# Performance work log

Measured on AMD Instinct MI355X. Metric: run time of the kernel, lower is better.

## Reference

```python
import jax, jax.numpy as jnp
import numpy as np

N_NODES = 50000
N_EDGES = 1600000
D = 128  # in_dim = hidden = out_dim = 128


def _gat_layer(x, W, b, aW, ab, src, dst, n_nodes):
    # fc: z = x @ W^T + b   (torch Linear convention, W:[out,in])
    z = x @ W.T + b                      # [N, d]
    d = z.shape[1]
    # attn_fc(concat(z_src, z_dst)) decomposed into per-node halves
    a_src = z @ aW[0, :d]                # [N]
    a_dst = z @ aW[0, d:]                # [N]
    e = jax.nn.leaky_relu(a_src[src] + a_dst[dst] + ab[0])  # [E], slope 0.01 (torch default)
    # segment softmax over incoming edges of each dst node
    m = jax.ops.segment_max(e, dst, num_segments=n_nodes)   # [N]
    ex = jnp.exp(e - m[dst])             # [E]
    s = jax.ops.segment_sum(ex, dst, num_segments=n_nodes)  # [N]
    alpha = ex / s[dst]                  # [E]
    # weighted scatter-sum of source features
    h = jax.ops.segment_sum(alpha[:, None] * z[src], dst, num_segments=n_nodes)  # [N, d]
    return h


def setup_inputs() -> dict:
    key = jax.random.key(0)
    ks = jax.random.split(key, 16)
    x = jax.random.normal(ks[0], (N_NODES, D), dtype=jnp.float32)
    src = jax.random.randint(ks[1], (N_EDGES,), 0, N_NODES, dtype=jnp.int32)
    dst = jax.random.randint(ks[2], (N_EDGES,), 0, N_NODES, dtype=jnp.int32)
    inp = {"x": x, "src": src, "dst": dst, "t": 0}
    # 3 GAT layers (128->128, 128->128, 128->128); xavier-ish scale
    for i in range(3):
        base = 3 + 4 * i
        inp[f"W{i}"] = jax.random.normal(ks[base], (D, D), dtype=jnp.float32) * (1.0 / np.sqrt(D))
        inp[f"b{i}"] = jnp.zeros((D,), dtype=jnp.float32)
        inp[f"aW{i}"] = jax.random.normal(ks[base + 1], (1, 2 * D), dtype=jnp.float32) * (1.0 / np.sqrt(2 * D))
        inp[f"ab{i}"] = jnp.zeros((1,), dtype=jnp.float32)
    return inp


def reference(x, src, dst, t, W0, b0, aW0, ab0, W1, b1, aW1, ab1, W2, b2, aW2, ab2):
    n = x.shape[0]
    h = _gat_layer(x, W0, b0, aW0, ab0, src, dst, n)
    h = jax.nn.relu(h)
    h = _gat_layer(h, W1, b1, aW1, ab1, src, dst, n)
    h = jax.nn.relu(h)
    h = _gat_layer(h, W2, b2, aW2, ab2, src, dst, n)
    return h
```

## Files before the change

### kernel.cpp

```cpp
#include <hip/hip_runtime.h>
#include <hip/hip_fp16.h>
#include <math.h>

#define DD 128
#define NBKT 391
#define P1CHUNK 4096
#define P2CAP 8192


__global__ __launch_bounds__(256) void fill_zero_i(int* p, int n) {
    int i = blockIdx.x * 256 + threadIdx.x;
    if (i < n) p[i] = 0;
}


__global__ __launch_bounds__(512) void p1hist_k(const int* __restrict__ dst, int* __restrict__ gcount, int E) {
    __shared__ int lh[NBKT];
    const int tid = threadIdx.x;
    for (int i = tid; i < NBKT; i += 512) lh[i] = 0;
    __syncthreads();
    const int blk0 = blockIdx.x * P1CHUNK;
    const int blkE = min(blk0 + P1CHUNK, E);
    int i0 = blk0 + tid * 8;
    if (i0 + 8 <= blkE) {
        int4 d0 = *reinterpret_cast<const int4*>(dst + i0);
        int4 d1 = *reinterpret_cast<const int4*>(dst + i0 + 4);
        atomicAdd(&lh[d0.x >> 7], 1); atomicAdd(&lh[d0.y >> 7], 1);
        atomicAdd(&lh[d0.z >> 7], 1); atomicAdd(&lh[d0.w >> 7], 1);
        atomicAdd(&lh[d1.x >> 7], 1); atomicAdd(&lh[d1.y >> 7], 1);
        atomicAdd(&lh[d1.z >> 7], 1); atomicAdd(&lh[d1.w >> 7], 1);
    } else {
        for (int j = 0; j < 8; ++j) {
            int i = i0 + j;
            if (i < blkE) atomicAdd(&lh[dst[i] >> 7], 1);
        }
    }
    __syncthreads();
    for (int i = tid; i < NBKT; i += 512)
        if (lh[i]) atomicAdd(&gcount[i], lh[i]);
}


__global__ __launch_bounds__(512) void p1scan_k(const int* __restrict__ gcount, int* __restrict__ bbase,
                                                int* __restrict__ bcur, int E) {
    __shared__ int tmp[512];
    int t = threadIdx.x;
    int v = (t < NBKT) ? gcount[t] : 0;
    tmp[t] = v;
    __syncthreads();
#pragma unroll
    for (int o = 1; o < 512; o <<= 1) {
        int add = (t >= o) ? tmp[t - o] : 0;
        __syncthreads();
        tmp[t] += add;
        __syncthreads();
    }
    if (t <= NBKT) {
        int ex = (t < NBKT) ? (tmp[t] - v) : E;
        bbase[t] = ex;
        if (t < NBKT) bcur[t] = ex;
    }
}


__global__ __launch_bounds__(512) void p1scatter_k(const int* __restrict__ src, const int* __restrict__ dst,
                                                   int* __restrict__ bcur, int2* __restrict__ bufA, int E) {
    __shared__ int lcnt[NBKT];
    __shared__ int lstart[512];
    __shared__ int blkb[NBKT];
    __shared__ int2 stage[P1CHUNK];
    const int tid = threadIdx.x;
    for (int i = tid; i < NBKT; i += 512) lcnt[i] = 0;
    __syncthreads();
    const int blk0 = blockIdx.x * P1CHUNK;
    const int blkE = min(blk0 + P1CHUNK, E);
    const int i0 = blk0 + tid * 8;

    int sv[8], dv[8], bn[8], rk[8], cntT = 0;
    if (i0 + 8 <= blkE) {
        int4 s0 = *reinterpret_cast<const int4*>(src + i0);
        int4 s1 = *reinterpret_cast<const int4*>(src + i0 + 4);
        int4 d0 = *reinterpret_cast<const int4*>(dst + i0);
        int4 d1 = *reinterpret_cast<const int4*>(dst + i0 + 4);
        sv[0] = s0.x; sv[1] = s0.y; sv[2] = s0.z; sv[3] = s0.w;
        sv[4] = s1.x; sv[5] = s1.y; sv[6] = s1.z; sv[7] = s1.w;
        dv[0] = d0.x; dv[1] = d0.y; dv[2] = d0.z; dv[3] = d0.w;
        dv[4] = d1.x; dv[5] = d1.y; dv[6] = d1.z; dv[7] = d1.w;
        cntT = 8;
    } else {
#pragma unroll
        for (int j = 0; j < 8; ++j) {
            int i = i0 + j;
            if (i < blkE) { sv[j] = src[i]; dv[j] = dst[i]; cntT = j + 1; }
        }
    }
#pragma unroll
    for (int j = 0; j < 8; ++j) {
        if (j < cntT) {
            bn[j] = dv[j] >> 7;
            rk[j] = atomicAdd(&lcnt[bn[j]], 1);
        }
    }
    __syncthreads();
    int v = (tid < NBKT) ? lcnt[tid] : 0;
    lstart[tid] = v;
    __syncthreads();
#pragma unroll
    for (int o = 1; o < 512; o <<= 1) {
        int add = (tid >= o) ? lstart[tid - o] : 0;
        __syncthreads();
        lstart[tid] += add;
        __syncthreads();
    }
    lstart[tid] -= v;
    __syncthreads();
    for (int i = tid; i < NBKT; i += 512)
        blkb[i] = lcnt[i] ? atomicAdd(&bcur[i], lcnt[i]) : 0;
#pragma unroll
    for (int j = 0; j < 8; ++j) {
        if (j < cntT) {
            int pos = lstart[bn[j]] + rk[j];
            stage[pos] = make_int2(sv[j], dv[j]);
        }
    }
    __syncthreads();
    const int cnt = blkE - blk0;
    for (int j = tid; j < cnt; j += 512) {
        int2 e = stage[j];
        int b = e.y >> 7;
        bufA[blkb[b] + (j - lstart[b])] = e;
    }
}


__global__ __launch_bounds__(512) void p2sort_k(const int2* __restrict__ bufA, const int* __restrict__ bbase,
                                                int* __restrict__ srcs, int* __restrict__ dstS) {
    __shared__ int h2[128];
    __shared__ int start2[128];
    __shared__ int cur2[128];
    __shared__ int ssrc[P2CAP];
    __shared__ int sdst[P2CAP];
    const int tid = threadIdx.x;
    const int b = blockIdx.x;
    const int base = bbase[b];
    const int cnt = bbase[b + 1] - base;
    for (int i = tid; i < 128; i += 512) h2[i] = 0;
    __syncthreads();
    for (int j = tid; j < cnt; j += 512)
        atomicAdd(&h2[bufA[base + j].y & 127], 1);
    __syncthreads();
    if (tid == 0) {
        int s = 0;
        for (int i = 0; i < 128; ++i) { start2[i] = s; cur2[i] = s; s += h2[i]; }
    }
    __syncthreads();
    for (int j = tid; j < cnt; j += 512) {
        int2 e = bufA[base + j];
        int p = atomicAdd(&cur2[e.y & 127], 1);
        ssrc[p] = e.x;
        sdst[p] = e.y;
    }
    __syncthreads();
    for (int j = tid; j < cnt; j += 512) {
        srcs[base + j] = ssrc[j];
        dstS[base + j] = sdst[j];
    }
}


__global__ __launch_bounds__(512) void off_k(const int* __restrict__ dstS, int* __restrict__ off, int N, int E) {
    int i = blockIdx.x * 512 + threadIdx.x;
    if (i >= E) return;
    int d = dstS[i];
    int p = (i == 0) ? -1 : dstS[i - 1];
    if (d != p)
        for (int n = p + 1; n <= d; ++n) off[n] = i;
    if (i == E - 1)
        for (int n = d + 1; n <= N; ++n) off[n] = E;
}


__global__ __launch_bounds__(512) void gemm_k(const float* __restrict__ X, const float* __restrict__ W,
                                              const float* __restrict__ B, const float* __restrict__ aW,
                                              __half* __restrict__ Zh, float* __restrict__ a_src,
                                              float* __restrict__ a_dst, int N) {
    __shared__ __align__(16) float xs[32][128];
    __shared__ __align__(16) float ws[32][128];
    const int tid = threadIdx.x;
    const int row0 = blockIdx.x * 128;
    const int cg = tid & 31;
    const int rg = tid >> 5;
    float acc[8][4];
#pragma unroll
    for (int i = 0; i < 8; ++i)
#pragma unroll
        for (int j = 0; j < 4; ++j) acc[i][j] = 0.f;

    for (int kc = 0; kc < DD; kc += 32) {
        {
            int r = tid >> 2;
            int k4 = (tid & 3) * 8;
            int gr = row0 + r;
            if (gr >= N) gr = N - 1;
            const float4* p = reinterpret_cast<const float4*>(X + (size_t)gr * DD + kc + k4);
            float4 v0 = p[0], v1 = p[1];
            xs[k4 + 0][r] = v0.x; xs[k4 + 1][r] = v0.y; xs[k4 + 2][r] = v0.z; xs[k4 + 3][r] = v0.w;
            xs[k4 + 4][r] = v1.x; xs[k4 + 5][r] = v1.y; xs[k4 + 6][r] = v1.z; xs[k4 + 7][r] = v1.w;
        }
        {
            int o = tid >> 2;
            int k8 = (tid & 3) * 8;
            const float4* p = reinterpret_cast<const float4*>(W + (size_t)o * DD + kc + k8);
            float4 v0 = p[0], v1 = p[1];
            ws[k8 + 0][o] = v0.x; ws[k8 + 1][o] = v0.y; ws[k8 + 2][o] = v0.z; ws[k8 + 3][o] = v0.w;
            ws[k8 + 4][o] = v1.x; ws[k8 + 5][o] = v1.y; ws[k8 + 6][o] = v1.z; ws[k8 + 7][o] = v1.w;
        }
        __syncthreads();
#pragma unroll
        for (int k = 0; k < 32; ++k) {
            const float4 wv = *reinterpret_cast<const float4*>(&ws[k][cg * 4]);
            const float4 xa = *reinterpret_cast<const float4*>(&xs[k][rg * 8]);
            const float4 xb = *reinterpret_cast<const float4*>(&xs[k][rg * 8 + 4]);
            float xr[8] = {xa.x, xa.y, xa.z, xa.w, xb.x, xb.y, xb.z, xb.w};
            float wr[4] = {wv.x, wv.y, wv.z, wv.w};
#pragma unroll
            for (int i = 0; i < 8; ++i)
#pragma unroll
                for (int j = 0; j < 4; ++j)
                    acc[i][j] = fmaf(xr[i], wr[j], acc[i][j]);
        }
        __syncthreads();
    }
    const int c0 = cg * 4;
    const float4 bv = *reinterpret_cast<const float4*>(B + c0);
    const float4 aw0 = *reinterpret_cast<const float4*>(aW + c0);
    const float4 aw1 = *reinterpret_cast<const float4*>(aW + DD + c0);
    float pa[8], pb[8];
#pragma unroll
    for (int i = 0; i < 8; ++i) {
        acc[i][0] += bv.x; acc[i][1] += bv.y; acc[i][2] += bv.z; acc[i][3] += bv.w;
        pa[i] = acc[i][0] * aw0.x + acc[i][1] * aw0.y + acc[i][2] * aw0.z + acc[i][3] * aw0.w;
        pb[i] = acc[i][0] * aw1.x + acc[i][1] * aw1.y + acc[i][2] * aw1.z + acc[i][3] * aw1.w;
    }
#pragma unroll
    for (int o = 1; o < 32; o <<= 1) {
#pragma unroll
        for (int i = 0; i < 8; ++i) {
            pa[i] += __shfl_xor(pa[i], o);
            pb[i] += __shfl_xor(pb[i], o);
        }
    }
    const int sl = c0 >> 5;
    const int cin = c0 & 31;
#pragma unroll
    for (int i = 0; i < 8; ++i) {
        int gr = row0 + rg * 8 + i;
        if (gr < N) {
            __half2 p0 = __floats2half2_rn(acc[i][0], acc[i][1]);
            __half2 p1 = __floats2half2_rn(acc[i][2], acc[i][3]);
            __half2* dst2 = reinterpret_cast<__half2*>(Zh + ((size_t)sl * N + gr) * 32 + cin);
            dst2[0] = p0;
            dst2[1] = p1;
            if (cg == 0) {
                a_src[gr] = pa[i];
                a_dst[gr] = pb[i];
            }
        }
    }
}


__global__ __launch_bounds__(256) void alpha_k(const float* __restrict__ a_src, const float* __restrict__ a_dst,
                                               const int* __restrict__ off, const int* __restrict__ srcs,
                                               const float* __restrict__ ab, unsigned* __restrict__ pairc, int N) {
    int node = blockIdx.x * 4 + (threadIdx.x >> 6);
    int lane = threadIdx.x & 63;
    if (node >= N) return;
    const int beg = off[node], end = off[node + 1];
    const int deg = end - beg;
    const float adn = a_dst[node] + ab[0];
    if (deg <= 64) {
        int i = beg + lane;
        float p = 0.f; int s = 0;
        if (i < end) {
            s = srcs[i];
            float e = a_src[s] + adn;
            e = (e > 0.f) ? e : 0.01f * e;
            p = __expf(e);
        }
        float psum = p;
#pragma unroll
        for (int o = 1; o < 64; o <<= 1) psum += __shfl_xor(psum, o);
        float inv = (deg > 0) ? 1.0f / psum : 0.0f;
        if (i < end) {
            unsigned ah = __half_as_ushort(__float2half(p * inv));
            pairc[i] = (ah << 16) | (unsigned)s;
        }
    } else {
        float psum = 0.f;
        for (int i = beg + lane; i < end; i += 64) {
            float e = a_src[srcs[i]] + adn;
            e = (e > 0.f) ? e : 0.01f * e;
            psum += __expf(e);
        }
#pragma unroll
        for (int o = 1; o < 64; o <<= 1) psum += __shfl_xor(psum, o);
        const float inv = 1.0f / psum;
        for (int i = beg + lane; i < end; i += 64) {
            int s = srcs[i];
            float e = a_src[s] + adn;
            e = (e > 0.f) ? e : 0.01f * e;
            unsigned ah = __half_as_ushort(__float2half(__expf(e) * inv));
            pairc[i] = (ah << 16) | (unsigned)s;
        }
    }
}


__global__ __launch_bounds__(256) void aggr_k(const __half* __restrict__ Zh, const unsigned* __restrict__ pairc,
                                              const int* __restrict__ off, float* __restrict__ H,
                                              int N, int do_relu) {
    const int slice = blockIdx.x & 3;
    const int lane = threadIdx.x & 63;
    const int wid = threadIdx.x >> 6;
    const int ng = lane >> 4;
    const int node = (blockIdx.x >> 2) * 16 + wid * 4 + ng;
    if (node >= N) return;
    const int eg = (lane >> 2) & 3;
    const int ql = lane & 3;
    const int beg = off[node], end = off[node + 1];
    const __half* Zs = Zh + (size_t)slice * N * 32 + ql * 8;

    float acc[8];
#pragma unroll
    for (int k = 0; k < 8; ++k) acc[k] = 0.f;

    int i = beg + eg;
    for (; i + 4 < end; i += 8) {
        unsigned w0 = pairc[i];
        unsigned w1 = pairc[i + 4];
        int s0 = (int)(w0 & 0xffffu);
        int s1 = (int)(w1 & 0xffffu);
        float a0 = __half2float(__ushort_as_half((unsigned short)(w0 >> 16)));
        float a1 = __half2float(__ushort_as_half((unsigned short)(w1 >> 16)));
        int4 r0 = *reinterpret_cast<const int4*>(Zs + (size_t)s0 * 32);
        int4 r1 = *reinterpret_cast<const int4*>(Zs + (size_t)s1 * 32);
        const __half* h0 = reinterpret_cast<const __half*>(&r0);
        const __half* h1 = reinterpret_cast<const __half*>(&r1);
#pragma unroll
        for (int k = 0; k < 8; ++k) acc[k] = fmaf(a0, __half2float(h0[k]), acc[k]);
#pragma unroll
        for (int k = 0; k < 8; ++k) acc[k] = fmaf(a1, __half2float(h1[k]), acc[k]);
    }
    if (i < end) {
        unsigned w0 = pairc[i];
        int s0 = (int)(w0 & 0xffffu);
        float a0 = __half2float(__ushort_as_half((unsigned short)(w0 >> 16)));
        int4 r0 = *reinterpret_cast<const int4*>(Zs + (size_t)s0 * 32);
        const __half* h0 = reinterpret_cast<const __half*>(&r0);
#pragma unroll
        for (int k = 0; k < 8; ++k) acc[k] = fmaf(a0, __half2float(h0[k]), acc[k]);
    }
#pragma unroll
    for (int o = 4; o <= 8; o <<= 1) {
#pragma unroll
        for (int k = 0; k < 8; ++k) acc[k] += __shfl_xor(acc[k], o);
    }
    if (eg == 0) {
#pragma unroll
        for (int k = 0; k < 8; ++k)
            if (do_relu) acc[k] = fmaxf(acc[k], 0.f);
        float* out = H + (size_t)node * DD + slice * 32 + ql * 8;
#pragma unroll
        for (int k = 0; k < 8; ++k)
            __builtin_nontemporal_store(acc[k], out + k);
    }
}


extern "C" void kernel_launch(void* const* d_in, const int* in_sizes, int n_in,
                              void* d_out, int out_size, void* d_ws, size_t ws_size,
                              hipStream_t stream) {
    const float* x  = (const float*)d_in[0];
    const int* src  = (const int*)d_in[1];
    const int* dst  = (const int*)d_in[2];
    const float* Wl[3]  = {(const float*)d_in[4],  (const float*)d_in[8],  (const float*)d_in[12]};
    const float* bl[3]  = {(const float*)d_in[5],  (const float*)d_in[9],  (const float*)d_in[13]};
    const float* aWl[3] = {(const float*)d_in[6],  (const float*)d_in[10], (const float*)d_in[14]};
    const float* abl[3] = {(const float*)d_in[7],  (const float*)d_in[11], (const float*)d_in[15]};
    const int N = in_sizes[0] / DD;
    const int E = in_sizes[1];

    char* p = (char*)d_ws;
    auto alloc = [&](size_t bytes) -> char* {
        char* r = p;
        p += (bytes + 255) & ~(size_t)255;
        return r;
    };
    __half* zh  = (__half*)alloc((size_t)N * DD * 2);
    float* hA   = (float*)alloc((size_t)N * DD * 4);
    float* hB   = (float*)alloc((size_t)N * DD * 4);
    float* asrc = (float*)alloc((size_t)N * 4);
    float* adst = (float*)alloc((size_t)N * 4);
    int* off    = (int*)alloc((size_t)(N + 1) * 4);
    int* srcs   = (int*)alloc((size_t)E * 4);
    unsigned* pairc = (unsigned*)alloc((size_t)E * 4);
    int* gcount = (int*)alloc(512 * 4);
    int* bbase  = (int*)alloc(512 * 4);
    int* bcur   = (int*)alloc(512 * 4);
    int2* bufA  = (int2*)hB;
    int* dstS   = (int*)hA;

    const int NBLK1 = (E + P1CHUNK - 1) / P1CHUNK;

    fill_zero_i<<<2, 256, 0, stream>>>(gcount, 512);
    p1hist_k<<<NBLK1, 512, 0, stream>>>(dst, gcount, E);
    p1scan_k<<<1, 512, 0, stream>>>(gcount, bbase, bcur, E);
    p1scatter_k<<<NBLK1, 512, 0, stream>>>(src, dst, bcur, bufA, E);
    p2sort_k<<<NBKT, 512, 0, stream>>>(bufA, bbase, srcs, dstS);
    off_k<<<(E + 511) / 512, 512, 0, stream>>>(dstS, off, N, E);

    const float* in = x;
    float* outs[3] = {hA, hB, (float*)d_out};
    const int node_blocks = (N + 3) / 4;
    const int aggr_blocks = 4 * ((N + 15) / 16);
    for (int l = 0; l < 3; ++l) {
        gemm_k<<<(N + 127) / 128, 512, 0, stream>>>(in, Wl[l], bl[l], aWl[l], zh, asrc, adst, N);
        alpha_k<<<node_blocks, 256, 0, stream>>>(asrc, adst, off, srcs, abl[l], pairc, N);
        aggr_k<<<aggr_blocks, 256, 0, stream>>>(zh, pairc, off, outs[l], N, (l < 2) ? 1 : 0);
        in = outs[l];
    }
}
```

Measured before the change: 314.2 us.

## Fuse offset computation into bucket sort and widen per-lane edge unroll in aggregation

The CSR offset computation moves into the second-stage sort kernel, which derives each node's offsets from the shared-memory sorted destinations. This removes the separate off_k launch and the global round trip of the sorted-destination array. Separately, the aggregation kernel now gives each node 8 lanes (2 edge groups) instead of 16 (4 edge groups) and issues four gathers per iteration. That doubles nodes per block, raises memory-level parallelism per lane and needs only one shuffle-reduction step, at the cost of more serial work per lane for high-degree nodes.

```diff
diff --git a/kernel.cpp b/kernel.cpp
--- a/kernel.cpp
+++ b/kernel.cpp
@@ -134,9 +134,8 @@
 
 
 __global__ __launch_bounds__(512) void p2sort_k(const int2* __restrict__ bufA, const int* __restrict__ bbase,
-                                                int* __restrict__ srcs, int* __restrict__ dstS) {
+                                                int* __restrict__ srcs, int* __restrict__ off, int N, int E) {
     __shared__ int h2[128];
-    __shared__ int start2[128];
     __shared__ int cur2[128];
     __shared__ int ssrc[P2CAP];
     __shared__ int sdst[P2CAP];
@@ -151,7 +150,7 @@
     __syncthreads();
     if (tid == 0) {
         int s = 0;
-        for (int i = 0; i < 128; ++i) { start2[i] = s; cur2[i] = s; s += h2[i]; }
+        for (int i = 0; i < 128; ++i) { cur2[i] = s; s += h2[i]; }
     }
     __syncthreads();
     for (int j = tid; j < cnt; j += 512) {
@@ -161,22 +160,19 @@
         sdst[p] = e.y;
     }
     __syncthreads();
+    const int n0 = b * 128;
+    const int n1 = min(n0 + 128, N);
     for (int j = tid; j < cnt; j += 512) {
         srcs[base + j] = ssrc[j];
-        dstS[base + j] = sdst[j];
-    }
-}
-
-
-__global__ __launch_bounds__(512) void off_k(const int* __restrict__ dstS, int* __restrict__ off, int N, int E) {
-    int i = blockIdx.x * 512 + threadIdx.x;
-    if (i >= E) return;
-    int d = dstS[i];
-    int p = (i == 0) ? -1 : dstS[i - 1];
-    if (d != p)
-        for (int n = p + 1; n <= d; ++n) off[n] = i;
-    if (i == E - 1)
-        for (int n = d + 1; n <= N; ++n) off[n] = E;
+        int d = sdst[j];
+        int p = (j == 0) ? (n0 - 1) : sdst[j - 1];
+        for (int n = p + 1; n <= d; ++n) off[n] = base + j;
+        if (j == cnt - 1)
+            for (int n = d + 1; n < n1; ++n) off[n] = base + cnt;
+    }
+    if (cnt == 0)
+        for (int n = n0 + tid; n < n1; n += 512) off[n] = base;
+    if (b == NBKT - 1 && tid == 0) off[N] = E;
 }
 
 
@@ -323,10 +319,10 @@
     const int slice = blockIdx.x & 3;
     const int lane = threadIdx.x & 63;
     const int wid = threadIdx.x >> 6;
-    const int ng = lane >> 4;
-    const int node = (blockIdx.x >> 2) * 16 + wid * 4 + ng;
+    const int ng = lane >> 3;
+    const int node = (blockIdx.x >> 2) * 32 + wid * 8 + ng;
     if (node >= N) return;
-    const int eg = (lane >> 2) & 3;
+    const int eg = (lane >> 2) & 1;
     const int ql = lane & 3;
     const int beg = off[node], end = off[node + 1];
     const __half* Zs = Zh + (size_t)slice * N * 32 + ql * 8;
@@ -336,23 +332,37 @@
     for (int k = 0; k < 8; ++k) acc[k] = 0.f;
 
     int i = beg + eg;
-    for (; i + 4 < end; i += 8) {
+    for (; i + 6 < end; i += 8) {
         unsigned w0 = pairc[i];
-        unsigned w1 = pairc[i + 4];
+        unsigned w1 = pairc[i + 2];
+        unsigned w2 = pairc[i + 4];
+        unsigned w3 = pairc[i + 6];
         int s0 = (int)(w0 & 0xffffu);
         int s1 = (int)(w1 & 0xffffu);
+        int s2 = (int)(w2 & 0xffffu);
+        int s3 = (int)(w3 & 0xffffu);
+        int4 r0 = *reinterpret_cast<const int4*>(Zs + (size_t)s0 * 32);
+        int4 r1 = *reinterpret_cast<const int4*>(Zs + (size_t)s1 * 32);
+        int4 r2 = *reinterpret_cast<const int4*>(Zs + (size_t)s2 * 32);
+        int4 r3 = *reinterpret_cast<const int4*>(Zs + (size_t)s3 * 32);
         float a0 = __half2float(__ushort_as_half((unsigned short)(w0 >> 16)));
         float a1 = __half2float(__ushort_as_half((unsigned short)(w1 >> 16)));
-        int4 r0 = *reinterpret_cast<const int4*>(Zs + (size_t)s0 * 32);
-        int4 r1 = *reinterpret_cast<const int4*>(Zs + (size_t)s1 * 32);
+        float a2 = __half2float(__ushort_as_half((unsigned short)(w2 >> 16)));
+        float a3 = __half2float(__ushort_as_half((unsigned short)(w3 >> 16)));
         const __half* h0 = reinterpret_cast<const __half*>(&r0);
         const __half* h1 = reinterpret_cast<const __half*>(&r1);
+        const __half* h2 = reinterpret_cast<const __half*>(&r2);
+        const __half* h3 = reinterpret_cast<const __half*>(&r3);
 #pragma unroll
         for (int k = 0; k < 8; ++k) acc[k] = fmaf(a0, __half2float(h0[k]), acc[k]);
 #pragma unroll
         for (int k = 0; k < 8; ++k) acc[k] = fmaf(a1, __half2float(h1[k]), acc[k]);
-    }
-    if (i < end) {
+#pragma unroll
+        for (int k = 0; k < 8; ++k) acc[k] = fmaf(a2, __half2float(h2[k]), acc[k]);
+#pragma unroll
+        for (int k = 0; k < 8; ++k) acc[k] = fmaf(a3, __half2float(h3[k]), acc[k]);
+    }
+    for (; i < end; i += 2) {
         unsigned w0 = pairc[i];
         int s0 = (int)(w0 & 0xffffu);
         float a0 = __half2float(__ushort_as_half((unsigned short)(w0 >> 16)));
@@ -362,10 +372,7 @@
         for (int k = 0; k < 8; ++k) acc[k] = fmaf(a0, __half2float(h0[k]), acc[k]);
     }
 #pragma unroll
-    for (int o = 4; o <= 8; o <<= 1) {
-#pragma unroll
-        for (int k = 0; k < 8; ++k) acc[k] += __shfl_xor(acc[k], o);
-    }
+    for (int k = 0; k < 8; ++k) acc[k] += __shfl_xor(acc[k], 4);
     if (eg == 0) {
 #pragma unroll
         for (int k = 0; k < 8; ++k)
@@ -409,7 +416,6 @@
     int* bbase  = (int*)alloc(512 * 4);
     int* bcur   = (int*)alloc(512 * 4);
     int2* bufA  = (int2*)hB;
-    int* dstS   = (int*)hA;
 
     const int NBLK1 = (E + P1CHUNK - 1) / P1CHUNK;
 
@@ -417,13 +423,12 @@
     p1hist_k<<<NBLK1, 512, 0, stream>>>(dst, gcount, E);
     p1scan_k<<<1, 512, 0, stream>>>(gcount, bbase, bcur, E);
     p1scatter_k<<<NBLK1, 512, 0, stream>>>(src, dst, bcur, bufA, E);
-    p2sort_k<<<NBKT, 512, 0, stream>>>(bufA, bbase, srcs, dstS);
-    off_k<<<(E + 511) / 512, 512, 0, stream>>>(dstS, off, N, E);
+    p2sort_k<<<NBKT, 512, 0, stream>>>(bufA, bbase, srcs, off, N, E);
 
     const float* in = x;
     float* outs[3] = {hA, hB, (float*)d_out};
     const int node_blocks = (N + 3) / 4;
-    const int aggr_blocks = 4 * ((N + 15) / 16);
+    const int aggr_blocks = 4 * ((N + 31) / 32);
     for (int l = 0; l < 3; ++l) {
         gemm_k<<<(N + 127) / 128, 512, 0, stream>>>(in, Wl[l], bl[l], aWl[l], zh, asrc, adst, N);
         alpha_k<<<node_blocks, 256, 0, stream>>>(asrc, adst, off, srcs, abl[l], pairc, N);
```

After: 312.8 us. Within noise of the previous version (-0.4%).

## Use fp16 MFMA GEMM with half activations and fuse offset build into sort

Applied to the files above, without the earlier changes.

The FP32 SIMT GEMM is replaced with an fp16 MFMA 16x16x32 kernel. Inputs are converted to half by new conversion kernels, and the intermediate layer outputs are now stored as half with ReLU fused in. The separate off_k kernel is removed: p2sort_k computes node offsets directly from its sorted shared buffer, which also drops the dstS global write. This cuts GEMM compute time and intermediate memory traffic, at the cost of lower precision in the inputs and activations and some extra conversion launches.

```diff
diff --git a/kernel.cpp b/kernel.cpp
--- a/kernel.cpp
+++ b/kernel.cpp
@@ -7,10 +7,45 @@
 #define P1CHUNK 4096
 #define P2CAP 8192
 
+typedef _Float16 half8 __attribute__((ext_vector_type(8)));
+typedef float floatx4 __attribute__((ext_vector_type(4)));
+
 
 __global__ __launch_bounds__(256) void fill_zero_i(int* p, int n) {
     int i = blockIdx.x * 256 + threadIdx.x;
     if (i < n) p[i] = 0;
+}
+
+
+__global__ __launch_bounds__(256) void cvt_k(const float* __restrict__ X, __half* __restrict__ Xh, int n8) {
+    int i = blockIdx.x * 256 + threadIdx.x;
+    if (i >= n8) return;
+    const float4* p = reinterpret_cast<const float4*>(X + (size_t)i * 8);
+    float4 v0 = p[0], v1 = p[1];
+    __half hv[8];
+    hv[0] = __float2half(v0.x); hv[1] = __float2half(v0.y);
+    hv[2] = __float2half(v0.z); hv[3] = __float2half(v0.w);
+    hv[4] = __float2half(v1.x); hv[5] = __float2half(v1.y);
+    hv[6] = __float2half(v1.z); hv[7] = __float2half(v1.w);
+    *reinterpret_cast<int4*>(Xh + (size_t)i * 8) = *reinterpret_cast<const int4*>(hv);
+}
+
+__global__ __launch_bounds__(256) void cvtw3_k(const float* __restrict__ W0, const float* __restrict__ W1,
+                                               const float* __restrict__ W2, __half* __restrict__ Wh3) {
+    int i = blockIdx.x * 256 + threadIdx.x;
+    if (i >= 2048) return;
+    const float* Ws[3] = {W0, W1, W2};
+#pragma unroll
+    for (int m = 0; m < 3; ++m) {
+        const float4* p = reinterpret_cast<const float4*>(Ws[m] + (size_t)i * 8);
+        float4 v0 = p[0], v1 = p[1];
+        __half hv[8];
+        hv[0] = __float2half(v0.x); hv[1] = __float2half(v0.y);
+        hv[2] = __float2half(v0.z); hv[3] = __float2half(v0.w);
+        hv[4] = __float2half(v1.x); hv[5] = __float2half(v1.y);
+        hv[6] = __float2half(v1.z); hv[7] = __float2half(v1.w);
+        *reinterpret_cast<int4*>(Wh3 + (size_t)m * 16384 + (size_t)i * 8) = *reinterpret_cast<const int4*>(hv);
+    }
 }
 
 
@@ -134,9 +169,8 @@
 
 
 __global__ __launch_bounds__(512) void p2sort_k(const int2* __restrict__ bufA, const int* __restrict__ bbase,
-                                                int* __restrict__ srcs, int* __restrict__ dstS) {
+                                                int* __restrict__ srcs, int* __restrict__ off, int N, int E) {
     __shared__ int h2[128];
-    __shared__ int start2[128];
     __shared__ int cur2[128];
     __shared__ int ssrc[P2CAP];
     __shared__ int sdst[P2CAP];
@@ -151,7 +185,7 @@
     __syncthreads();
     if (tid == 0) {
         int s = 0;
-        for (int i = 0; i < 128; ++i) { start2[i] = s; cur2[i] = s; s += h2[i]; }
+        for (int i = 0; i < 128; ++i) { cur2[i] = s; s += h2[i]; }
     }
     __syncthreads();
     for (int j = tid; j < cnt; j += 512) {
@@ -161,109 +195,85 @@
         sdst[p] = e.y;
     }
     __syncthreads();
+    const int n0 = b * 128;
+    const int n1 = min(n0 + 128, N);
     for (int j = tid; j < cnt; j += 512) {
         srcs[base + j] = ssrc[j];
-        dstS[base + j] = sdst[j];
-    }
-}
-
-
-__global__ __launch_bounds__(512) void off_k(const int* __restrict__ dstS, int* __restrict__ off, int N, int E) {
-    int i = blockIdx.x * 512 + threadIdx.x;
-    if (i >= E) return;
-    int d = dstS[i];
-    int p = (i == 0) ? -1 : dstS[i - 1];
-    if (d != p)
-        for (int n = p + 1; n <= d; ++n) off[n] = i;
-    if (i == E - 1)
-        for (int n = d + 1; n <= N; ++n) off[n] = E;
-}
-
-
-__global__ __launch_bounds__(512) void gemm_k(const float* __restrict__ X, const float* __restrict__ W,
+        int d = sdst[j];
+        int p = (j == 0) ? (n0 - 1) : sdst[j - 1];
+        for (int n = p + 1; n <= d; ++n) off[n] = base + j;
+        if (j == cnt - 1)
+            for (int n = d + 1; n < n1; ++n) off[n] = base + cnt;
+    }
+    if (cnt == 0)
+        for (int n = n0 + tid; n < n1; n += 512) off[n] = base;
+    if (b == NBKT - 1 && tid == 0) off[N] = E;
+}
+
+
+__global__ __launch_bounds__(256) void gemm_k(const __half* __restrict__ Xh, const __half* __restrict__ Wh,
                                               const float* __restrict__ B, const float* __restrict__ aW,
                                               __half* __restrict__ Zh, float* __restrict__ a_src,
                                               float* __restrict__ a_dst, int N) {
-    __shared__ __align__(16) float xs[32][128];
-    __shared__ __align__(16) float ws[32][128];
     const int tid = threadIdx.x;
-    const int row0 = blockIdx.x * 128;
-    const int cg = tid & 31;
-    const int rg = tid >> 5;
-    float acc[8][4];
-#pragma unroll
-    for (int i = 0; i < 8; ++i)
-#pragma unroll
-        for (int j = 0; j < 4; ++j) acc[i][j] = 0.f;
-
-    for (int kc = 0; kc < DD; kc += 32) {
-        {
-            int r = tid >> 2;
-            int k4 = (tid & 3) * 8;
-            int gr = row0 + r;
-            if (gr >= N) gr = N - 1;
-            const float4* p = reinterpret_cast<const float4*>(X + (size_t)gr * DD + kc + k4);
-            float4 v0 = p[0], v1 = p[1];
-            xs[k4 + 0][r] = v0.x; xs[k4 + 1][r] = v0.y; xs[k4 + 2][r] = v0.z; xs[k4 + 3][r] = v0.w;
-            xs[k4 + 4][r] = v1.x; xs[k4 + 5][r] = v1.y; xs[k4 + 6][r] = v1.z; xs[k4 + 7][r] = v1.w;
-        }
-        {
-            int o = tid >> 2;
-            int k8 = (tid & 3) * 8;
-            const float4* p = reinterpret_cast<const float4*>(W + (size_t)o * DD + kc + k8);
-            float4 v0 = p[0], v1 = p[1];
-            ws[k8 + 0][o] = v0.x; ws[k8 + 1][o] = v0.y; ws[k8 + 2][o] = v0.z; ws[k8 + 3][o] = v0.w;
-            ws[k8 + 4][o] = v1.x; ws[k8 + 5][o] = v1.y; ws[k8 + 6][o] = v1.z; ws[k8 + 7][o] = v1.w;
-        }
-        __syncthreads();
-#pragma unroll
-        for (int k = 0; k < 32; ++k) {
-            const float4 wv = *reinterpret_cast<const float4*>(&ws[k][cg * 4]);
-            const float4 xa = *reinterpret_cast<const float4*>(&xs[k][rg * 8]);
-            const float4 xb = *reinterpret_cast<const float4*>(&xs[k][rg * 8 + 4]);
-            float xr[8] = {xa.x, xa.y, xa.z, xa.w, xb.x, xb.y, xb.z, xb.w};
-            float wr[4] = {wv.x, wv.y, wv.z, wv.w};
-#pragma unroll
-            for (int i = 0; i < 8; ++i)
-#pragma unroll
-                for (int j = 0; j < 4; ++j)
-                    acc[i][j] = fmaf(xr[i], wr[j], acc[i][j]);
-        }
-        __syncthreads();
-    }
-    const int c0 = cg * 4;
-    const float4 bv = *reinterpret_cast<const float4*>(B + c0);
-    const float4 aw0 = *reinterpret_cast<const float4*>(aW + c0);
-    const float4 aw1 = *reinterpret_cast<const float4*>(aW + DD + c0);
-    float pa[8], pb[8];
-#pragma unroll
-    for (int i = 0; i < 8; ++i) {
-        acc[i][0] += bv.x; acc[i][1] += bv.y; acc[i][2] += bv.z; acc[i][3] += bv.w;
-        pa[i] = acc[i][0] * aw0.x + acc[i][1] * aw0.y + acc[i][2] * aw0.z + acc[i][3] * aw0.w;
-        pb[i] = acc[i][0] * aw1.x + acc[i][1] * aw1.y + acc[i][2] * aw1.z + acc[i][3] * aw1.w;
-    }
-#pragma unroll
-    for (int o = 1; o < 32; o <<= 1) {
-#pragma unroll
-        for (int i = 0; i < 8; ++i) {
-            pa[i] += __shfl_xor(pa[i], o);
-            pb[i] += __shfl_xor(pb[i], o);
-        }
-    }
-    const int sl = c0 >> 5;
-    const int cin = c0 & 31;
-#pragma unroll
-    for (int i = 0; i < 8; ++i) {
-        int gr = row0 + rg * 8 + i;
-        if (gr < N) {
-            __half2 p0 = __floats2half2_rn(acc[i][0], acc[i][1]);
-            __half2 p1 = __floats2half2_rn(acc[i][2], acc[i][3]);
-            __half2* dst2 = reinterpret_cast<__half2*>(Zh + ((size_t)sl * N + gr) * 32 + cin);
-            dst2[0] = p0;
-            dst2[1] = p1;
-            if (cg == 0) {
-                a_src[gr] = pa[i];
-                a_dst[gr] = pb[i];
+    const int wid = tid >> 6;
+    const int lane = tid & 63;
+    const int cl = lane & 15;
+    const int kg = lane >> 4;
+    const int row0 = blockIdx.x * 64 + wid * 16;
+    int rowA = row0 + cl;
+    if (rowA >= N) rowA = N - 1;
+
+    floatx4 acc[8];
+#pragma unroll
+    for (int t = 0; t < 8; ++t) acc[t] = {0.f, 0.f, 0.f, 0.f};
+
+    const _Float16* Xp = reinterpret_cast<const _Float16*>(Xh);
+    const _Float16* Wp = reinterpret_cast<const _Float16*>(Wh);
+#pragma unroll
+    for (int kk = 0; kk < 4; ++kk) {
+        const int kb = kk * 32 + kg * 8;
+        half8 av = *reinterpret_cast<const half8*>(Xp + (size_t)rowA * 128 + kb);
+#pragma unroll
+        for (int t = 0; t < 8; ++t) {
+            half8 bv = *reinterpret_cast<const half8*>(Wp + (size_t)(t * 16 + cl) * 128 + kb);
+            acc[t] = __builtin_amdgcn_mfma_f32_16x16x32_f16(av, bv, acc[t], 0, 0, 0);
+        }
+    }
+    float pa[4] = {0.f, 0.f, 0.f, 0.f}, pb[4] = {0.f, 0.f, 0.f, 0.f};
+#pragma unroll
+    for (int t = 0; t < 8; ++t) {
+        const int c = t * 16 + cl;
+        const float bc = B[c];
+        const float w0 = aW[c];
+        const float w1 = aW[128 + c];
+        const int sl = c >> 5;
+        const int cin = c & 31;
+#pragma unroll
+        for (int j = 0; j < 4; ++j) {
+            float z = acc[t][j] + bc;
+            pa[j] = fmaf(z, w0, pa[j]);
+            pb[j] = fmaf(z, w1, pb[j]);
+            int grow = row0 + kg * 4 + j;
+            if (grow < N)
+                Zh[((size_t)sl * N + grow) * 32 + cin] = __float2half(z);
+        }
+    }
+#pragma unroll
+    for (int o = 1; o < 16; o <<= 1) {
+#pragma unroll
+        for (int j = 0; j < 4; ++j) {
+            pa[j] += __shfl_xor(pa[j], o);
+            pb[j] += __shfl_xor(pb[j], o);
+        }
+    }
+    if (cl == 0) {
+#pragma unroll
+        for (int j = 0; j < 4; ++j) {
+            int grow = row0 + kg * 4 + j;
+            if (grow < N) {
+                a_src[grow] = pa[j];
+                a_dst[grow] = pb[j];
             }
         }
     }
@@ -318,8 +328,8 @@
 
 
 __global__ __launch_bounds__(256) void aggr_k(const __half* __restrict__ Zh, const unsigned* __restrict__ pairc,
-                                              const int* __restrict__ off, float* __restrict__ H,
-                                              int N, int do_relu) {
+                                              const int* __restrict__ off, float* __restrict__ Hf,
+                                              __half* __restrict__ Hh, int N) {
     const int slice = blockIdx.x & 3;
     const int lane = threadIdx.x & 63;
     const int wid = threadIdx.x >> 6;
@@ -367,13 +377,18 @@
         for (int k = 0; k < 8; ++k) acc[k] += __shfl_xor(acc[k], o);
     }
     if (eg == 0) {
-#pragma unroll
-        for (int k = 0; k < 8; ++k)
-            if (do_relu) acc[k] = fmaxf(acc[k], 0.f);
-        float* out = H + (size_t)node * DD + slice * 32 + ql * 8;
-#pragma unroll
-        for (int k = 0; k < 8; ++k)
-            __builtin_nontemporal_store(acc[k], out + k);
+        if (Hh) {
+            __half hv[8];
+#pragma unroll
+            for (int k = 0; k < 8; ++k) hv[k] = __float2half(fmaxf(acc[k], 0.f));
+            *reinterpret_cast<int4*>(Hh + (size_t)node * DD + slice * 32 + ql * 8) =
+                *reinterpret_cast<const int4*>(hv);
+        } else {
+            float* out = Hf + (size_t)node * DD + slice * 32 + ql * 8;
+#pragma unroll
+            for (int k = 0; k < 8; ++k)
+                __builtin_nontemporal_store(acc[k], out + k);
+        }
     }
 }
 
@@ -397,9 +412,10 @@
         p += (bytes + 255) & ~(size_t)255;
         return r;
     };
+    __half* Wh3 = (__half*)alloc(3 * 16384 * 2);
+    __half* XhA = (__half*)alloc((size_t)N * DD * 2);
+    __half* XhB = (__half*)alloc((size_t)N * DD * 2);
     __half* zh  = (__half*)alloc((size_t)N * DD * 2);
-    float* hA   = (float*)alloc((size_t)N * DD * 4);
-    float* hB   = (float*)alloc((size_t)N * DD * 4);
     float* asrc = (float*)alloc((size_t)N * 4);
     float* adst = (float*)alloc((size_t)N * 4);
     int* off    = (int*)alloc((size_t)(N + 1) * 4);
@@ -408,8 +424,7 @@
     int* gcount = (int*)alloc(512 * 4);
     int* bbase  = (int*)alloc(512 * 4);
     int* bcur   = (int*)alloc(512 * 4);
-    int2* bufA  = (int2*)hB;
-    int* dstS   = (int*)hA;
+    int2* bufA  = (int2*)alloc((size_t)E * 8);
 
     const int NBLK1 = (E + P1CHUNK - 1) / P1CHUNK;
 
@@ -417,17 +432,22 @@
     p1hist_k<<<NBLK1, 512, 0, stream>>>(dst, gcount, E);
     p1scan_k<<<1, 512, 0, stream>>>(gcount, bbase, bcur, E);
     p1scatter_k<<<NBLK1, 512, 0, stream>>>(src, dst, bcur, bufA, E);
-    p2sort_k<<<NBKT, 512, 0, stream>>>(bufA, bbase, srcs, dstS);
-    off_k<<<(E + 511) / 512, 512, 0, stream>>>(dstS, off, N, E);
-
-    const float* in = x;
-    float* outs[3] = {hA, hB, (float*)d_out};
+    p2sort_k<<<NBKT, 512, 0, stream>>>(bufA, bbase, srcs, off, N, E);
+    cvtw3_k<<<8, 256, 0, stream>>>(Wl[0], Wl[1], Wl[2], Wh3);
+    const int n8 = N * DD / 8;
+    cvt_k<<<(n8 + 255) / 256, 256, 0, stream>>>(x, XhA, n8);
+
     const int node_blocks = (N + 3) / 4;
     const int aggr_blocks = 4 * ((N + 15) / 16);
+    const int gemm_blocks = (N + 63) / 64;
+
+    __half* xin[3]  = {XhA, XhB, XhA};
+    __half* hout[3] = {XhB, XhA, nullptr};
     for (int l = 0; l < 3; ++l) {
-        gemm_k<<<(N + 127) / 128, 512, 0, stream>>>(in, Wl[l], bl[l], aWl[l], zh, asrc, adst, N);
+        gemm_k<<<gemm_blocks, 256, 0, stream>>>(xin[l], Wh3 + (size_t)l * 16384, bl[l], aWl[l],
+                                                zh, asrc, adst, N);
         alpha_k<<<node_blocks, 256, 0, stream>>>(asrc, adst, off, srcs, abl[l], pairc, N);
-        aggr_k<<<aggr_blocks, 256, 0, stream>>>(zh, pairc, off, outs[l], N, (l < 2) ? 1 : 0);
-        in = outs[l];
-    }
-}
+        aggr_k<<<aggr_blocks, 256, 0, stream>>>(zh, pairc, off,
+                                                (l == 2) ? (float*)d_out : nullptr, hout[l], N);
+    }
+}
```

Result: faster. 297.7 us (-5.3%).
